# Performance work log

Measured on AMD Instinct MI355X. Metric: run time of the kernel, lower is better.

Reference implementation:

```python
import jax, jax.numpy as jnp
import numpy as np

EPS = 1e-5
N_HEADS = 32
TEMPERATURE = 1.0


def _inorm(x, g, b):
    # InstanceNorm2d (affine): normalize over H,W per (N, C)
    m = jnp.mean(x, axis=(-2, -1), keepdims=True)
    v = jnp.var(x, axis=(-2, -1), keepdims=True)
    return (x - m) * jax.lax.rsqrt(v + EPS) * g + b


def _resample(x, out_hw):
    # Fourier (spectral) resampling, matching neuraloperator's resample for skips
    H, W = x.shape[-2:]
    Ho, Wo = out_hw
    if (H, W) == (Ho, Wo):
        return x
    xf = jnp.fft.rfft2(x, norm='forward')
    kh = min(H, Ho) // 2
    kw = min(W // 2 + 1, Wo // 2 + 1)
    of = jnp.zeros(x.shape[:-2] + (Ho, Wo // 2 + 1), dtype=xf.dtype)
    of = of.at[..., :kh, :kw].set(xf[..., :kh, :kw])
    of = of.at[..., -kh:, :kw].set(xf[..., -kh:, :kw])
    return jnp.fft.irfft2(of, s=(Ho, Wo), norm='forward')


def _spec_conv(x, w, out_hw):
    # w: [2(pos/neg rows), in, out, m1, m2, 2(re/im)]; fft_norm='forward'
    m1, m2 = w.shape[3], w.shape[4]
    Ho, Wo = out_hw
    wc = w[..., 0] + 1j * w[..., 1]  # [2, in, out, m1, m2]
    xf = jnp.fft.rfft2(x, norm='forward')  # [B, Cin, H, W//2+1]
    top = jnp.einsum('bimn,iomn->bomn', xf[:, :, :m1, :m2], wc[0])
    bot = jnp.einsum('bimn,iomn->bomn', xf[:, :, -m1:, :m2], wc[1])
    of = jnp.zeros((x.shape[0], w.shape[2], Ho, Wo // 2 + 1), dtype=xf.dtype)
    of = of.at[:, :, :m1, :m2].set(top)
    of = of.at[:, :, -m1:, :m2].set(bot)
    return jnp.fft.irfft2(of, s=(Ho, Wo), norm='forward')


def _fno_layer(x, w, ws, bs, out_hw, norm_gb=None, act=False):
    # one FNOBlock layer: spectral conv + linear (1x1) skip, optional instance norm + gelu
    skip = jnp.einsum('bchw,oc->bohw', x, ws) + bs[None, :, None, None]
    skip = _resample(skip, out_hw)
    fno = _spec_conv(x, w, out_hw)
    if norm_gb is not None:
        fno = _inorm(fno, norm_gb[0], norm_gb[1])
    y = fno + skip
    if act:
        y = jax.nn.gelu(y, approximate=False)  # torch F.gelu default = exact erf
    return y


def _forward(x, wK, wKs, bKs, wQ, wQs, bQs, wV, wVs, bVs, wP, wPs, bPs,
             wM0, wM0s, bM0s, wM1, wM1s, bM1s, norm_g, norm_b):
    B, T, H, W = x.shape  # token_codimension == 1 -> tokens T == channels
    xa = x.reshape(B * T, 1, H, W)
    xa_n = _inorm(xa, norm_g[0], norm_b[0])  # self.norm1
    # K, Q at half resolution (output_scaling_factor = 1/scale, scale = 2); V at full res
    k = _fno_layer(xa_n, wK, wKs, bKs, (H // 2, W // 2))
    q = _fno_layer(xa_n, wQ, wQs, bQs, (H // 2, W // 2))
    v = _fno_layer(xa_n, wV, wVs, bVs, (H, W))

    def to_seq(z):
        h, w = z.shape[-2:]
        z = z.reshape(B, T, N_HEADS, 1, h, w).transpose(0, 2, 1, 3, 4, 5)
        return z.reshape(B, N_HEADS, T, h * w)  # d = head_codim = 1

    qs, ks, vs = to_seq(q), to_seq(k), to_seq(v)
    scores = jnp.einsum('bhtd,bhsd->bhts', qs, ks) / (np.sqrt(ks.shape[-1]).astype(np.float32) * TEMPERATURE)
    attn_w = jax.nn.softmax(scores, axis=-1)
    out = jnp.einsum('bhts,bhsd->bhtd', attn_w, vs)  # [B, heads, T, H*W]
    out = out.reshape(B, N_HEADS, T, 1, H, W).transpose(0, 2, 1, 3, 4, 5)
    out = out.reshape(B * T, N_HEADS, H, W)
    # proj: n_heads*head_codim != token_codim -> FNO projection back to 1 channel
    projd = _fno_layer(out, wP, wPs, bPs, (H, W))
    attention = _inorm(projd + xa, norm_g[1], norm_b[1])  # attention_normalizer
    an = _inorm(attention, norm_g[2], norm_b[2])  # self.norm2
    # permutation-equivariant mixer: 2 FNO layers, instance_norm, gelu between layers
    m = _fno_layer(an, wM0, wM0s, bM0s, (H, W), (norm_g[3], norm_b[3]), act=True)
    m = _fno_layer(m, wM1, wM1s, bM1s, (H, W), (norm_g[4], norm_b[4]), act=False)
    output = _inorm(m, norm_g[5], norm_b[5]) + attention  # mixer_out_normalizer + residual
    return output.reshape(B, T, H, W)


def setup_inputs() -> dict:
    key = jax.random.key(0)
    ks = jax.random.split(key, 16)
    B, T, H, W, heads = 2, 32, 128, 128, 32

    def rn(k, shape, s=1.0):
        return jax.random.normal(k, shape, jnp.float32) * s

    inp = {'x': rn(ks[0], (B, T, H, W))}
    for i, nm in enumerate(['K', 'Q', 'V']):
        inp['w' + nm] = rn(ks[1 + 3 * i], (2, 1, heads, 16, 16, 2), 1.0 / heads)
        inp['w' + nm + 's'] = rn(ks[2 + 3 * i], (heads, 1), 1.0)
        inp['b' + nm + 's'] = jnp.zeros((heads,), jnp.float32)
    inp['wP'] = rn(ks[10], (2, heads, 1, 32, 32, 2), 1.0 / heads)
    inp['wPs'] = rn(ks[11], (1, heads), 1.0 / heads)
    inp['bPs'] = jnp.zeros((1,), jnp.float32)
    inp['wM0'] = rn(ks[12], (2, 1, 1, 32, 32, 2), 1.0)
    inp['wM0s'] = rn(ks[13], (1, 1), 1.0)
    inp['bM0s'] = jnp.zeros((1,), jnp.float32)
    inp['wM1'] = rn(ks[14], (2, 1, 1, 32, 32, 2), 1.0)
    inp['wM1s'] = rn(ks[15], (1, 1), 1.0)
    inp['bM1s'] = jnp.zeros((1,), jnp.float32)
    inp['norm_g'] = jnp.ones((6,), jnp.float32)
    inp['norm_b'] = jnp.zeros((6,), jnp.float32)
    return inp


def reference(x, wK, wKs, bKs, wQ, wQs, bQs, wV, wVs, bVs, wP, wPs, bPs,
              wM0, wM0s, bM0s, wM1, wM1s, bM1s, norm_g, norm_b):
    return _forward(x, wK, wKs, bKs, wQ, wQs, bQs, wV, wVs, bVs, wP, wPs, bPs,
                    wM0, wM0s, bM0s, wM1, wM1s, bM1s, norm_g, norm_b)
```

## Files before the change

kernel.cpp:

```cpp
#include <hip/hip_runtime.h>
#include <math.h>


#define EPSV 1e-5f
#define PI2 6.283185307179586f

typedef float2 cf;

__device__ __forceinline__ cf cmul(cf a, cf b){ return make_float2(a.x*b.x - a.y*b.y, a.x*b.y + a.y*b.x); }
__device__ __forceinline__ cf ldc(const float* p){ return make_float2(p[0], p[1]); }
__device__ __forceinline__ void stc(float* p, cf v){ p[0]=v.x; p[1]=v.y; }

__device__ __forceinline__ void init_tw(cf* tw, int N, float dir){
  for (int j = threadIdx.x; j < N; j += blockDim.x){
    float s, c; sincosf(dir * PI2 * (float)j / (float)N, &s, &c);
    tw[j] = make_float2(c, s);
  }
}

__device__ void breduce2(float& a, float& b){
  __shared__ float sha[8], shb[8];
  for (int off = 32; off > 0; off >>= 1){
    a += __shfl_down(a, off, 64);
    b += __shfl_down(b, off, 64);
  }
  int w = threadIdx.x >> 6, lane = threadIdx.x & 63;
  int nw = (blockDim.x + 63) >> 6;
  if (lane == 0){ sha[w] = a; shb[w] = b; }
  __syncthreads();
  if (threadIdx.x == 0){
    for (int i = 1; i < nw; ++i){ a += sha[i]; b += shb[i]; }
    sha[0] = a; shb[0] = b;
  }
  __syncthreads();
  a = sha[0]; b = shb[0];
  __syncthreads();
}

__device__ __forceinline__ cf kq_mode(const float* w, int o, int kh, int kw){
  if (kw < 16){
    if (kh < 16)  return ldc(w + ((o*16+kh)*16+kw)*2);
    if (kh >= 48) return ldc(w + (((32+o)*16+(kh-48))*16+kw)*2);
  }
  return make_float2(0.f,0.f);
}

__global__ __launch_bounds__(256) void k_gamma_xstats(
                      const float* __restrict__ wQ, const float* __restrict__ wQs,
                      const float* __restrict__ bQs,
                      const float* __restrict__ wK, const float* __restrict__ wKs,
                      const float* __restrict__ bKs,
                      const float* __restrict__ x, const float* __restrict__ ng,
                      const float* __restrict__ nb,
                      float* __restrict__ gam, float* __restrict__ gcons,
                      float* __restrict__ stats, float* __restrict__ normAB){
  if (blockIdx.x >= 32){
    int n = blockIdx.x - 32;
    const float* im = x + n*16384;
    float s=0.f, s2=0.f;
    for (int i=threadIdx.x;i<16384;i+=256){ float v=im[i]; s+=v; s2=fmaf(v,v,s2); }
    breduce2(s,s2);
    if (threadIdx.x==0){
      float m = s*(1.f/16384.f), var = s2*(1.f/16384.f)-m*m;
      float A = rsqrtf(var+EPSV)*ng[0];
      normAB[n*2]=A; normAB[n*2+1]=nb[0]-m*A;
    }
    return;
  }
  int o = blockIdx.x;
  if (o==0){ for (int i=threadIdx.x;i<512;i+=256) stats[i]=0.f; }
  float sQ=wQs[o], sK=wKs[o];
  for (int m = threadIdx.x; m < 2112; m += 256){
    int kh = m/33, kw = m-kh*33;
    cf g;
    if (kw == 0){
      int mh = (64-kh)&63;
      cf qp = kq_mode(wQ,o,kh,0);  qp.x += sQ;
      cf qm = kq_mode(wQ,o,mh,0);  qm.x += sQ;
      cf qt = make_float2(0.5f*(qp.x+qm.x), 0.5f*(qp.y-qm.y));
      cf kp = kq_mode(wK,o,kh,0);  kp.x += sK;
      cf km = kq_mode(wK,o,mh,0);  km.x += sK;
      cf kt = make_float2(0.5f*(kp.x+km.x), 0.5f*(kp.y-km.y));
      g = make_float2(64.f*(qt.x*kt.x + qt.y*kt.y), 64.f*(qt.y*kt.x - qt.x*kt.y));
    } else if (kw == 32){
      g = make_float2(64.f*sQ*sK, 0.f);
    } else {
      cf q = kq_mode(wQ,o,kh,kw); q.x += sQ;
      cf k = kq_mode(wK,o,kh,kw); k.x += sK;
      g = make_float2(128.f*(q.x*k.x + q.y*k.y), 128.f*(q.y*k.x - q.x*k.y));
    }
    stc(gam + (o*2112+m)*2, g);
  }
  if (threadIdx.x == 0){
    float qt0 = sQ + kq_mode(wQ,o,0,0).x;
    float kt0 = sK + kq_mode(wK,o,0,0).x;
    gcons[o]    = 64.f*bKs[o]*qt0;
    gcons[32+o] = 64.f*bQs[o]*kt0;
    gcons[64+o] = 64.f*bQs[o]*bKs[o];
  }
}

__global__ __launch_bounds__(256) void k_rfft_row_x(const float* __restrict__ x, const float* __restrict__ normAB,
                                                    float* __restrict__ Cw){
  __shared__ float tile[16][128];
  __shared__ cf tw[128];
  init_tw(tw, 128, -1.f);
  int n = blockIdx.x, h0 = blockIdx.y*16;
  float A = normAB[n*2], Bc = normAB[n*2+1];
  for (int i=threadIdx.x;i<2048;i+=256) tile[i>>7][i&127] = fmaf(x[n*16384 + h0*128 + i], A, Bc);
  __syncthreads();
  for (int i=threadIdx.x;i<1024;i+=256){
    int hl=i>>6, w=i&63;
    float a=tile[hl][w], b=tile[hl][w+64];
    tile[hl][w]=a+b; tile[hl][w+64]=a-b;
  }
  __syncthreads();
  int hl = threadIdx.x >> 4, kws = threadIdx.x & 15;
  for (int kw=kws; kw<33; kw+=16){
    int sel = (kw&1)? 64 : 0;
    float re=0.f, im=0.f; int idx=0;
    for (int w=0;w<64;++w){
      float v=tile[hl][sel+w]; cf t=tw[idx];
      re=fmaf(v,t.x,re); im=fmaf(v,t.y,im);
      idx=(idx+kw)&127;
    }
    float* d = Cw + (((n*128)+(h0+hl))*33 + kw)*2;
    d[0]=re*(1.f/16384.f); d[1]=im*(1.f/16384.f);
  }
}

__global__ __launch_bounds__(256) void k_fcol(const float* __restrict__ Cw, float* __restrict__ F){
  __shared__ cf col[4][128];
  __shared__ cf tw[128];
  init_tw(tw, 128, -1.f);
  int n = blockIdx.x, kwb = blockIdx.y*4;
  for (int i=threadIdx.x;i<512;i+=256){
    int kwl=i>>7, h=i&127; int kw=kwb+kwl;
    col[kwl][h] = (kw<33) ? ldc(Cw + ((n*128+h)*33+kw)*2) : make_float2(0.f,0.f);
  }
  __syncthreads();
  {
    int i = threadIdx.x;
    int kwl = i>>6, h = i&63;
    cf a = col[kwl][h], b = col[kwl][h+64];
    col[kwl][h]    = make_float2(a.x+b.x, a.y+b.y);
    col[kwl][h+64] = make_float2(a.x-b.x, a.y-b.y);
  }
  __syncthreads();
  int r = threadIdx.x & 63, kwl = threadIdx.x >> 6;
  int kw = kwb + kwl;
  if (kw >= 33) return;
  int R = (r<32)? r : r+64;
  int sel = (r&1)? 64 : 0;
  float re=0.f, im=0.f; int idx=0;
  for (int j=0;j<64;++j){
    cf v=col[kwl][sel+j]; cf t=tw[idx];
    re = fmaf(v.x,t.x,re); re = fmaf(-v.y,t.y,re);
    im = fmaf(v.x,t.y,im); im = fmaf(v.y,t.x,im);
    idx=(idx+R)&127;
  }
  stc(F + ((n*64+r)*33+kw)*2, make_float2(re,im));
}

__global__ __launch_bounds__(256) void k_score(const float* __restrict__ F, const float* __restrict__ gam,
                                               float* __restrict__ scoreP){
  __shared__ float2 Esh[66][33];
  __shared__ float2 gsh[4][66];
  int mk = blockIdx.x, b = blockIdx.y, og = blockIdx.z;
  int m0 = mk*66;
  int t = threadIdx.x >> 3, s4 = (threadIdx.x & 7) << 2;
  for (int i = threadIdx.x; i < 2112; i += 256){
    int tt = i/66, j = i - tt*66;
    int m = m0 + j;
    int kh = m/33, kw = m - kh*33;
    const float* Fb = F + (b*32+tt)*4224;
    float2 v;
    if (kw < 32) v = *(const float2*)(Fb + (kh*33+kw)*2);
    else {
      int mh = (64-kh)&63;
      float2 a = *(const float2*)(Fb + (kh*33+32)*2);
      float2 c = *(const float2*)(Fb + (mh*33+32)*2);
      v = make_float2(0.5f*(a.x+c.x), 0.5f*(a.y-c.y));
    }
    Esh[j][tt] = v;
  }
  for (int i = threadIdx.x; i < 264; i += 256){
    int ol = i/66, j = i - ol*66;
    gsh[ol][j] = *(const float2*)(gam + ((og*4+ol)*2112 + m0 + j)*2);
  }
  __syncthreads();
  float acc[4][4];
  #pragma unroll
  for (int a=0;a<4;++a) for (int k=0;k<4;++k) acc[a][k]=0.f;
  #pragma unroll 2
  for (int j=0;j<66;++j){
    float2 et = Esh[j][t];
    float2 e0 = Esh[j][s4+0];
    float2 e1 = Esh[j][s4+1];
    float2 e2 = Esh[j][s4+2];
    float2 e3 = Esh[j][s4+3];
    #pragma unroll
    for (int ol=0;ol<4;++ol){
      float2 g = gsh[ol][j];
      float a  = g.x*et.x - g.y*et.y;
      float bb = g.x*et.y + g.y*et.x;
      acc[ol][0] = fmaf(a,e0.x,fmaf(bb,e0.y,acc[ol][0]));
      acc[ol][1] = fmaf(a,e1.x,fmaf(bb,e1.y,acc[ol][1]));
      acc[ol][2] = fmaf(a,e2.x,fmaf(bb,e2.y,acc[ol][2]));
      acc[ol][3] = fmaf(a,e3.x,fmaf(bb,e3.y,acc[ol][3]));
    }
  }
  #pragma unroll
  for (int ol=0;ol<4;++ol){
    int o = og*4+ol;
    float* sp = scoreP + (((mk*2+b)*32+o)*32 + t)*32 + s4;
    sp[0]=acc[ol][0]; sp[1]=acc[ol][1]; sp[2]=acc[ol][2]; sp[3]=acc[ol][3];
  }
}

__global__ __launch_bounds__(1024) void k_softmax(float* __restrict__ attn, const float* __restrict__ F,
                                                const float* __restrict__ gcons, const float* __restrict__ scoreP){
  __shared__ float Ssh[32][33];
  int b = blockIdx.x, o = blockIdx.y;
  int t = threadIdx.x >> 5, s = threadIdx.x & 31;
  float c0=gcons[o], c1=gcons[32+o], c2=gcons[64+o];
  float sc = c0*F[(b*32+t)*4224] + c1*F[(b*32+s)*4224] + c2;
  #pragma unroll 8
  for (int p=0;p<32;++p) sc += scoreP[(((p*2+b)*32+o)*32 + t)*32 + s];
  Ssh[t][s] = sc;
  __syncthreads();
  float mx = -1e30f;
  for (int ss=0;ss<32;++ss) mx = fmaxf(mx, Ssh[t][ss]);
  float e = expf(sc - mx);
  __syncthreads();
  Ssh[t][s] = e;
  __syncthreads();
  float sum = 0.f;
  for (int ss=0;ss<32;++ss) sum += Ssh[t][ss];
  attn[(b*32+o)*1024 + t*32 + s] = e/sum;
}

__device__ __forceinline__ cf wcV_col0(const float* wV, int o, int fr){
  if (fr < 16)  return ldc(wV + ((o*16+fr)*16)*2);
  if (fr >= 112) return ldc(wV + (((32+o)*16+(fr-112))*16)*2);
  return make_float2(0.f,0.f);
}

__global__ __launch_bounds__(256) void k_pmode(const float* __restrict__ F, const float* __restrict__ attn,
                        const float* __restrict__ wV, const float* __restrict__ wVs,
                        const float* __restrict__ wP, const float* __restrict__ wPs,
                        float* __restrict__ Pm){
  __shared__ float att[32][8][32];
  __shared__ cf Fsh[32][32];
  __shared__ cf dsh[32][32];
  int b = blockIdx.x, mh = blockIdx.y, tg = blockIdx.z;
  int fr = mh<32 ? mh : mh+64;
  int half = (mh>=32)?1:0, mr = mh&31;
  for (int i=threadIdx.x; i<8192; i+=256){
    int o = i>>8, r = i&255;
    att[o][r>>5][r&31] = attn[(b*32+o)*1024 + tg*256 + r];
  }
  for (int i=threadIdx.x; i<1024; i+=256){
    int s=i>>5, kw=i&31;
    Fsh[s][kw] = ldc(F + (((b*32+s)*64+mh)*33+kw)*2);
  }
  for (int i=threadIdx.x; i<1024; i+=256){
    int o=i>>5, kw=i&31;
    cf wp = ldc(wP + (((half*32+o)*32+mr)*32+kw)*2);
    cf bP = make_float2(wPs[o]+wp.x, wp.y);
    cf aV = make_float2(wVs[o], 0.f);
    if (kw==0){
      cf w1 = wcV_col0(wV,o,fr);
      cf w2 = wcV_col0(wV,o,(128-fr)&127);
      aV.x += 0.5f*(w1.x + w2.x);
      aV.y += 0.5f*(w1.y - w2.y);
    } else if (kw<16){
      if (fr<16){ cf wv=ldc(wV + ((o*16+fr)*16+kw)*2); aV.x+=wv.x; aV.y+=wv.y; }
      else if (fr>=112){ cf wv=ldc(wV + (((32+o)*16+(fr-112))*16+kw)*2); aV.x+=wv.x; aV.y+=wv.y; }
    }
    cf c = cmul(bP, aV);
    c.x -= wPs[o]*wVs[o];
    dsh[o][kw]=c;
  }
  __syncthreads();
  int tl = threadIdx.x>>5, kw = threadIdx.x&31;
  float ax=0.f, ay=0.f;
  for (int o=0;o<32;++o){
    float er=0.f, ei=0.f;
    #pragma unroll
    for (int s4=0;s4<32;s4+=4){
      float4 a4 = *(const float4*)&att[o][tl][s4];
      cf f0=Fsh[s4][kw], f1=Fsh[s4+1][kw], f2=Fsh[s4+2][kw], f3=Fsh[s4+3][kw];
      er=fmaf(a4.x,f0.x,er); ei=fmaf(a4.x,f0.y,ei);
      er=fmaf(a4.y,f1.x,er); ei=fmaf(a4.y,f1.y,ei);
      er=fmaf(a4.z,f2.x,er); ei=fmaf(a4.z,f2.y,ei);
      er=fmaf(a4.w,f3.x,er); ei=fmaf(a4.w,f3.y,ei);
    }
    cf d = dsh[o][kw];
    ax += d.x*er - d.y*ei;
    ay += d.x*ei + d.y*er;
  }
  int t = tg*8+tl;
  stc(Pm + ((b*32+t)*2048 + mh*32+kw)*2, make_float2(ax,ay));
}

__global__ __launch_bounds__(256) void k_zmix(const float* __restrict__ x, const float* __restrict__ Pm,
                        const float* __restrict__ attn, const float* __restrict__ normAB,
                        const float* __restrict__ wVs, const float* __restrict__ wPs,
                        const float* __restrict__ wP, const float* __restrict__ bPs,
                        const float* __restrict__ bVs,
                        float* __restrict__ z, float* __restrict__ stats){
  __shared__ cf Pmsh[64][33];
  __shared__ cf PmAsh[16][33];
  __shared__ float Mrow[32];
  __shared__ float cpart[33];
  __shared__ float consts;
  __shared__ cf tw[128];
  init_tw(tw, 128, 1.f);
  int n = blockIdx.x, b = n>>5, t = n&31, hb = blockIdx.y*8;
  for (int i=threadIdx.x;i<2048;i+=256)
    Pmsh[i>>5][i&31] = ldc(Pm + (n*2048 + i)*2);
  if (threadIdx.x < 32){
    int s = threadIdx.x;
    float a=0.f;
    for (int o=0;o<32;++o) a = fmaf(attn[(b*32+o)*1024 + t*32 + s], wVs[o]*wPs[o], a);
    float AxS = normAB[(b*32+s)*2], BcS = normAB[(b*32+s)*2+1];
    Mrow[s] = fmaf(a, AxS, (s==t)?1.f:0.f);
    cpart[s] = a*BcS;
  } else if (threadIdx.x == 32){
    float dcx = bPs[0];
    for (int o=0;o<32;++o){
      cf wp = ldc(wP + (o*1024)*2);
      dcx += (wPs[o]+wp.x)*bVs[o];
    }
    cpart[32] = dcx;
  }
  __syncthreads();
  if (threadIdx.x == 0){
    float c=0.f;
    for (int i=0;i<33;++i) c += cpart[i];
    consts = c;
  }
  {
    int bl = threadIdx.x>>5, kw = threadIdx.x&31;
    int h = hb + bl;
    float ser=0.f, sei=0.f, sor=0.f, soi=0.f;
    int s2h = (2*h)&127;
    int idx = 0;
    for (int khi=0;khi<32;khi+=2){
      cf v=Pmsh[khi][kw]; cf tt=tw[idx];
      ser += v.x*tt.x - v.y*tt.y; sei += v.x*tt.y + v.y*tt.x;
      idx=(idx+s2h)&127;
    }
    idx = (96*h)&127;
    for (int khi=32;khi<64;khi+=2){
      cf v=Pmsh[khi][kw]; cf tt=tw[idx];
      ser += v.x*tt.x - v.y*tt.y; sei += v.x*tt.y + v.y*tt.x;
      idx=(idx+s2h)&127;
    }
    idx = h&127;
    for (int khi=1;khi<32;khi+=2){
      cf v=Pmsh[khi][kw]; cf tt=tw[idx];
      sor += v.x*tt.x - v.y*tt.y; soi += v.x*tt.y + v.y*tt.x;
      idx=(idx+s2h)&127;
    }
    idx = (97*h)&127;
    for (int khi=33;khi<64;khi+=2){
      cf v=Pmsh[khi][kw]; cf tt=tw[idx];
      sor += v.x*tt.x - v.y*tt.y; soi += v.x*tt.y + v.y*tt.x;
      idx=(idx+s2h)&127;
    }
    PmAsh[bl][kw]   = make_float2(ser+sor, sei+soi);
    PmAsh[8+bl][kw] = make_float2(ser-sor, sei-soi);
  }
  __syncthreads();
  float cst = consts;
  float s1=0.f, s2=0.f;
  const float* xb = x + b*32*16384;
  {
    int hl = threadIdx.x>>4, wg = threadIdx.x&15;
    int w0 = wg*4;
    int gh = (hl<8)? hb+hl : hb+(hl-8)+64;
    int off = gh*128;
    float Se[4], So[4];
    #pragma unroll
    for (int j=0;j<4;++j){
      int w = w0+j;
      int s2w = (2*w)&127;
      float se=0.f, so=0.f;
      int idx=0;
      for (int kwp=0;kwp<16;++kwp){
        cf v = PmAsh[hl][2*kwp]; cf tt=tw[idx];
        float term = v.x*tt.x - v.y*tt.y;
        se += (kwp? 2.f:1.f)*term;
        idx=(idx+s2w)&127;
      }
      idx = w&127;
      for (int kwp=0;kwp<16;++kwp){
        cf v = PmAsh[hl][2*kwp+1]; cf tt=tw[idx];
        so += 2.f*(v.x*tt.x - v.y*tt.y);
        idx=(idx+s2w)&127;
      }
      Se[j]=se; So[j]=so;
    }
    float mixa[4]={0,0,0,0}, mixb[4]={0,0,0,0};
    for (int s=0;s<32;++s){
      float m = Mrow[s];
      float4 xa = *(const float4*)(xb + s*16384 + off + w0);
      float4 xc = *(const float4*)(xb + s*16384 + off + w0 + 64);
      mixa[0]=fmaf(m,xa.x,mixa[0]); mixa[1]=fmaf(m,xa.y,mixa[1]);
      mixa[2]=fmaf(m,xa.z,mixa[2]); mixa[3]=fmaf(m,xa.w,mixa[3]);
      mixb[0]=fmaf(m,xc.x,mixb[0]); mixb[1]=fmaf(m,xc.y,mixb[1]);
      mixb[2]=fmaf(m,xc.z,mixb[2]); mixb[3]=fmaf(m,xc.w,mixb[3]);
    }
    float oa[4], ob[4];
    #pragma unroll
    for (int j=0;j<4;++j){
      oa[j] = cst + Se[j] + So[j] + mixa[j];
      ob[j] = cst + Se[j] - So[j] + mixb[j];
      s1 += oa[j]+ob[j];
      s2 += oa[j]*oa[j] + ob[j]*ob[j];
    }
    *(float4*)(z + n*16384 + off + w0)      = make_float4(oa[0],oa[1],oa[2],oa[3]);
    *(float4*)(z + n*16384 + off + w0 + 64) = make_float4(ob[0],ob[1],ob[2],ob[3]);
  }
  breduce2(s1,s2);
  if (threadIdx.x==0){ atomicAdd(&stats[n*2],s1); atomicAdd(&stats[n*2+1],s2); }
}

__global__ __launch_bounds__(256) void k_rfft_row_an(const float* __restrict__ z, const float* __restrict__ statsZ,
                              const float* __restrict__ ng, const float* __restrict__ nb,
                              float* __restrict__ Tm){
  __shared__ float tile[16][128];
  __shared__ cf tw[128];
  init_tw(tw,128,-1.f);
  int n=blockIdx.x, h0=blockIdx.y*16;
  float S=statsZ[n*2], S2=statsZ[n*2+1];
  float mz=S*(1.f/16384.f), vz=S2*(1.f/16384.f)-mz*mz;
  float az=rsqrtf(vz+EPSV);
  float g1=ng[1], g2=ng[2], b2v=nb[2];
  float vat = g1*g1*vz*az*az;
  float C1 = az*g1*rsqrtf(vat+EPSV)*g2;
  float Dc = b2v - mz*C1;
  for (int i=threadIdx.x;i<2048;i+=256)
    tile[i>>7][i&127] = fmaf(z[n*16384+h0*128+i], C1, Dc);
  __syncthreads();
  for (int i=threadIdx.x;i<1024;i+=256){
    int hl=i>>6, w=i&63;
    float a=tile[hl][w], b=tile[hl][w+64];
    tile[hl][w]=a+b; tile[hl][w+64]=a-b;
  }
  __syncthreads();
  for (int i=threadIdx.x;i<512;i+=256){
    int hl=i>>5, kw=i&31;
    int sel = (kw&1)? 64 : 0;
    float re=0.f,im=0.f; int idx=0;
    for (int w=0;w<64;++w){
      float v=tile[hl][sel+w]; cf t=tw[idx];
      re=fmaf(v,t.x,re); im=fmaf(v,t.y,im);
      idx=(idx+kw)&127;
    }
    float* d = Tm + ((n*128+h0+hl)*32+kw)*2;
    d[0]=re*(1.f/16384.f); d[1]=im*(1.f/16384.f);
  }
}

__global__ __launch_bounds__(256) void k_colpair(const float* __restrict__ Tm, const float* __restrict__ wM,
                                                 float* __restrict__ Am){
  __shared__ cf Tsh[128][9];
  __shared__ cf Gsh[64][9];
  __shared__ cf tw[128];
  init_tw(tw,128,-1.f);
  int n = blockIdx.x, kw8 = blockIdx.y*8;
  for (int i=threadIdx.x;i<1024;i+=256){
    int h=i>>3, kwl=i&7;
    Tsh[h][kwl] = ldc(Tm + ((n*128+h)*32 + kw8+kwl)*2);
  }
  __syncthreads();
  for (int i=threadIdx.x;i<512;i+=256){
    int h=i>>3, kwl=i&7;
    cf a=Tsh[h][kwl], b=Tsh[h+64][kwl];
    Tsh[h][kwl]    = make_float2(a.x+b.x, a.y+b.y);
    Tsh[h+64][kwl] = make_float2(a.x-b.x, a.y-b.y);
  }
  __syncthreads();
  {
    int kwl = threadIdx.x&7, base = threadIdx.x>>3;
    for (int r=0;r<2;++r){
      int khi = r*32 + base;
      int khF = (khi<32)? khi : khi+64;
      int sel = (khi&1)? 64 : 0;
      float re=0.f, im=0.f; int idx=0;
      for (int j=0;j<64;++j){
        cf v=Tsh[sel+j][kwl]; cf t=tw[idx];
        re += v.x*t.x - v.y*t.y; im += v.x*t.y + v.y*t.x;
        idx=(idx+khF)&127;
      }
      int half=(khi>=32)?1:0, mr=khi&31;
      cf wv = ldc(wM + ((half*32+mr)*32 + kw8+kwl)*2);
      Gsh[khi][kwl] = cmul(make_float2(re,im), wv);
    }
  }
  __syncthreads();
  {
    int kwl = threadIdx.x&7, base = threadIdx.x>>3;
    for (int r=0;r<2;++r){
      int h = r*32 + base;
      float ser=0.f, sei=0.f, sor=0.f, soi=0.f;
      int s2h = (2*h)&127;
      int idx=0;
      for (int khi=0;khi<32;khi+=2){
        cf v=Gsh[khi][kwl]; cf t=tw[idx];
        ser += v.x*t.x + v.y*t.y; sei += v.y*t.x - v.x*t.y;
        idx=(idx+s2h)&127;
      }
      idx=(96*h)&127;
      for (int khi=32;khi<64;khi+=2){
        cf v=Gsh[khi][kwl]; cf t=tw[idx];
        ser += v.x*t.x + v.y*t.y; sei += v.y*t.x - v.x*t.y;
        idx=(idx+s2h)&127;
      }
      idx=h&127;
      for (int khi=1;khi<32;khi+=2){
        cf v=Gsh[khi][kwl]; cf t=tw[idx];
        sor += v.x*t.x + v.y*t.y; soi += v.y*t.x - v.x*t.y;
        idx=(idx+s2h)&127;
      }
      idx=(97*h)&127;
      for (int khi=33;khi<64;khi+=2){
        cf v=Gsh[khi][kwl]; cf t=tw[idx];
        sor += v.x*t.x + v.y*t.y; soi += v.y*t.x - v.x*t.y;
        idx=(idx+s2h)&127;
      }
      stc(Am + ((n*128+h)*32 + kw8+kwl)*2,    make_float2(ser+sor, sei+soi));
      stc(Am + ((n*128+h+64)*32 + kw8+kwl)*2, make_float2(ser-sor, sei-soi));
    }
  }
}

__global__ __launch_bounds__(256) void k_mirfft_row(const float* __restrict__ Am, float* __restrict__ out,
                                                    float* __restrict__ stats){
  __shared__ cf rowA[16][33];
  __shared__ cf tw[128];
  init_tw(tw,128,1.f);
  int n=blockIdx.x, h0=blockIdx.y*16;
  for (int i=threadIdx.x;i<512;i+=256){
    int hl=i>>5, kw=i&31;
    rowA[hl][kw] = ldc(Am + ((n*128+h0+hl)*32+kw)*2);
  }
  __syncthreads();
  float s=0.f,s2=0.f;
  for (int i=threadIdx.x;i<1024;i+=256){
    int hl=i>>6, w=i&63;
    int s2w = (2*w)&127;
    float se=0.f, so=0.f;
    int idx=0;
    for (int kwp=0;kwp<16;++kwp){
      cf v=rowA[hl][2*kwp]; cf t=tw[idx];
      float term=v.x*t.x-v.y*t.y;
      se += (kwp? 2.f:1.f)*term;
      idx=(idx+s2w)&127;
    }
    idx = w&127;
    for (int kwp=0;kwp<16;++kwp){
      cf v=rowA[hl][2*kwp+1]; cf t=tw[idx];
      so += 2.f*(v.x*t.x-v.y*t.y);
      idx=(idx+s2w)&127;
    }
    float oa = se+so, ob = se-so;
    out[n*16384+(h0+hl)*128+w]    = oa;
    out[n*16384+(h0+hl)*128+w+64] = ob;
    s+=oa+ob; s2 += oa*oa + ob*ob;
  }
  breduce2(s,s2);
  if (threadIdx.x==0){ atomicAdd(&stats[n*2],s); atomicAdd(&stats[n*2+1],s2); }
}

__global__ __launch_bounds__(256) void k_m0_rfft_row(const float* __restrict__ fno, const float* __restrict__ z,
                              const float* __restrict__ stats0, const float* __restrict__ statsZ,
                              const float* __restrict__ ng, const float* __restrict__ nb,
                              const float* __restrict__ wM0s, const float* __restrict__ bM0s,
                              float* __restrict__ m0out, float* __restrict__ Tm){
  __shared__ float tile[16][128];
  __shared__ cf tw[128];
  init_tw(tw,128,-1.f);
  int n=blockIdx.x, h0=blockIdx.y*16;
  float S0=stats0[n*2], S02=stats0[n*2+1];
  float m0m=S0*(1.f/16384.f), v0=S02*(1.f/16384.f)-m0m*m0m;
  float A0=rsqrtf(v0+EPSV)*ng[3];
  float B0=nb[3]-m0m*A0;
  float Sz=statsZ[n*2], Sz2=statsZ[n*2+1];
  float mz=Sz*(1.f/16384.f), vz=Sz2*(1.f/16384.f)-mz*mz;
  float az=rsqrtf(vz+EPSV);
  float g1=ng[1], g2=ng[2];
  float vat=g1*g1*vz*az*az;
  float C1=az*g1*rsqrtf(vat+EPSV)*g2;
  float Dc=nb[2]-mz*C1;
  float ws_=wM0s[0], bs_=bM0s[0];
  for (int i=threadIdx.x;i<2048;i+=256){
    int gi = n*16384 + h0*128 + i;
    float nf = fmaf(fno[gi], A0, B0);
    float an = fmaf(z[gi], C1, Dc);
    float pre = nf + fmaf(ws_, an, bs_);
    float gv = 0.5f*pre*(1.f+erff(pre*0.70710678118654752f));
    tile[i>>7][i&127]=gv;
    m0out[gi]=gv;
  }
  __syncthreads();
  for (int i=threadIdx.x;i<1024;i+=256){
    int hl=i>>6, w=i&63;
    float a=tile[hl][w], b=tile[hl][w+64];
    tile[hl][w]=a+b; tile[hl][w+64]=a-b;
  }
  __syncthreads();
  for (int i=threadIdx.x;i<512;i+=256){
    int hl=i>>5, kw=i&31;
    int sel = (kw&1)? 64:0;
    float re=0.f,im=0.f; int idx=0;
    for (int w=0;w<64;++w){
      float v=tile[hl][sel+w]; cf t=tw[idx];
      re=fmaf(v,t.x,re); im=fmaf(v,t.y,im);
      idx=(idx+kw)&127;
    }
    float* d = Tm + ((n*128+h0+hl)*32+kw)*2;
    d[0]=re*(1.f/16384.f); d[1]=im*(1.f/16384.f);
  }
}

__global__ __launch_bounds__(256) void k_m1_mix(const float* fno1, const float* __restrict__ m0,
                         const float* __restrict__ stats1, const float* __restrict__ ng, const float* __restrict__ nb,
                         const float* __restrict__ wM1s, const float* __restrict__ bM1s,
                         float* m1out, float* __restrict__ stats2){
  int n=blockIdx.x, h0=blockIdx.y*16;
  float S=stats1[n*2], S2v=stats1[n*2+1];
  float m1m=S*(1.f/16384.f), v1=S2v*(1.f/16384.f)-m1m*m1m;
  float A1=rsqrtf(v1+EPSV)*ng[4];
  float Bc1=nb[4]-m1m*A1;
  float ws_=wM1s[0], bs_=bM1s[0];
  float s=0.f,s2=0.f;
  for (int i=threadIdx.x;i<2048;i+=256){
    int gi=n*16384+h0*128+i;
    float v = fmaf(fno1[gi],A1,Bc1) + fmaf(ws_,m0[gi],bs_);
    m1out[gi]=v;
    s+=v; s2=fmaf(v,v,s2);
  }
  breduce2(s,s2);
  if (threadIdx.x==0){ atomicAdd(&stats2[n*2],s); atomicAdd(&stats2[n*2+1],s2); }
}

__global__ __launch_bounds__(256) void k_final(const float* __restrict__ m1, const float* __restrict__ z,
                        const float* __restrict__ stats2, const float* __restrict__ statsZ,
                        const float* __restrict__ ng, const float* __restrict__ nb,
                        float* __restrict__ out){
  int n=blockIdx.x, h0=blockIdx.y*16;
  float S=stats2[n*2], S2v=stats2[n*2+1];
  float mm=S*(1.f/16384.f), vv=S2v*(1.f/16384.f)-mm*mm;
  float A2=rsqrtf(vv+EPSV)*ng[5];
  float B2c=nb[5]-mm*A2;
  float Sz=statsZ[n*2], Sz2=statsZ[n*2+1];
  float mz=Sz*(1.f/16384.f), vz=Sz2*(1.f/16384.f)-mz*mz;
  float Az=rsqrtf(vz+EPSV)*ng[1];
  float Bz=nb[1]-mz*Az;
  for (int i=threadIdx.x;i<2048;i+=256){
    int gi=n*16384+h0*128+i;
    out[gi] = fmaf(m1[gi],A2,B2c) + fmaf(z[gi],Az,Bz);
  }
}

extern "C" void kernel_launch(void* const* d_in, const int* in_sizes, int n_in,
                              void* d_out, int out_size, void* d_ws, size_t ws_size,
                              hipStream_t stream){
  (void)in_sizes; (void)n_in; (void)out_size; (void)ws_size;
  const float* x   = (const float*)d_in[0];
  const float* wK  = (const float*)d_in[1];
  const float* wKs = (const float*)d_in[2];
  const float* bKs = (const float*)d_in[3];
  const float* wQ  = (const float*)d_in[4];
  const float* wQs = (const float*)d_in[5];
  const float* bQs = (const float*)d_in[6];
  const float* wV  = (const float*)d_in[7];
  const float* wVs = (const float*)d_in[8];
  const float* bVs = (const float*)d_in[9];
  const float* wP  = (const float*)d_in[10];
  const float* wPs = (const float*)d_in[11];
  const float* bPs = (const float*)d_in[12];
  const float* wM0 = (const float*)d_in[13];
  const float* wM0s= (const float*)d_in[14];
  const float* bM0s= (const float*)d_in[15];
  const float* wM1 = (const float*)d_in[16];
  const float* wM1s= (const float*)d_in[17];
  const float* bM1s= (const float*)d_in[18];
  const float* ng  = (const float*)d_in[19];
  const float* nb  = (const float*)d_in[20];
  float* out = (float*)d_out;
  float* ws  = (float*)d_ws;

  float* F      = ws;
  float* Cw     = F + 270336;
  float* scoreP = Cw + 540672;
  float* attn   = scoreP + 2097152;
  float* stats  = attn + 65536;
  float* Pm     = stats + 512;
  float* gcons  = Pm + 262144;
  float* gam    = gcons + 128;
  float* normAB = gam + 135168;
  float* z      = normAB + 128;
  float* m0b    = z + 1048576;
  float* fx     = m0b + 1048576;
  float* Tm     = fx + 1048576;
  float* Am     = Tm + 524288;
  float* statsZ = stats;
  float* stats0 = stats + 128;
  float* stats1 = stats + 256;
  float* stats2 = stats + 384;

  k_gamma_xstats<<<96,256,0,stream>>>(wQ,wQs,bQs, wK,wKs,bKs, x, ng, nb, gam, gcons, stats, normAB);
  k_rfft_row_x<<<dim3(64,8),256,0,stream>>>(x, normAB, Cw);
  k_fcol<<<dim3(64,9),256,0,stream>>>(Cw, F);
  k_score<<<dim3(32,2,8),256,0,stream>>>(F, gam, scoreP);
  k_softmax<<<dim3(2,32),1024,0,stream>>>(attn, F, gcons, scoreP);
  k_pmode<<<dim3(2,64,4),256,0,stream>>>(F, attn, wV, wVs, wP, wPs, Pm);
  k_zmix<<<dim3(64,8),256,0,stream>>>(x, Pm, attn, normAB, wVs, wPs, wP, bPs, bVs, z, statsZ);
  k_rfft_row_an<<<dim3(64,8),256,0,stream>>>(z, statsZ, ng, nb, Tm);
  k_colpair<<<dim3(64,4),256,0,stream>>>(Tm, wM0, Am);
  k_mirfft_row<<<dim3(64,8),256,0,stream>>>(Am, fx, stats0);
  k_m0_rfft_row<<<dim3(64,8),256,0,stream>>>(fx, z, stats0, statsZ, ng, nb, wM0s, bM0s, m0b, Tm);
  k_colpair<<<dim3(64,4),256,0,stream>>>(Tm, wM1, Am);
  k_mirfft_row<<<dim3(64,8),256,0,stream>>>(Am, fx, stats1);
  k_m1_mix<<<dim3(64,8),256,0,stream>>>(fx, m0b, stats1, ng, nb, wM1s, bM1s, fx, stats2);
  k_final<<<dim3(64,8),256,0,stream>>>(fx, z, stats2, statsZ, ng, nb, out);
}
```

Baseline: 261.3 us.

## Fuse forward 2D FFT, fold row FFT into zmix, compute final norm stats analytically

Merges the row and column forward FFTs into a single 1024-thread kernel per image that keeps the intermediate in shared memory, so the Cw workspace round trip goes away. The row DFT of z moves into k_zmix, and the instance-norm affine is applied in the spectral domain inside k_colpair, which removes k_rfft_row_an. The k_m1_mix pass is dropped by deriving the second norm's mean and variance from sums of f1 and m0 plus a cross term gathered in the existing passes. This cuts launches and global traffic, but k_fwd2d runs only 64 blocks, so GPU occupancy is low, and the algebraic variance formula may lose some precision.

```diff
diff --git a/kernel.cpp b/kernel.cpp
--- a/kernel.cpp
+++ b/kernel.cpp
@@ -19,7 +19,7 @@
 }
 
 __device__ void breduce2(float& a, float& b){
-  __shared__ float sha[8], shb[8];
+  __shared__ float sha[16], shb[16];
   for (int off = 32; off > 0; off >>= 1){
     a += __shfl_down(a, off, 64);
     b += __shfl_down(b, off, 64);
@@ -68,7 +68,7 @@
     return;
   }
   int o = blockIdx.x;
-  if (o==0){ for (int i=threadIdx.x;i<512;i+=256) stats[i]=0.f; }
+  if (o==0){ for (int i=threadIdx.x;i<640;i+=256) stats[i]=0.f; }
   float sQ=wQs[o], sK=wKs[o];
   for (int m = threadIdx.x; m < 2112; m += 256){
     int kh = m/33, kw = m-kh*33;
@@ -100,66 +100,54 @@
   }
 }
 
-__global__ __launch_bounds__(256) void k_rfft_row_x(const float* __restrict__ x, const float* __restrict__ normAB,
-                                                    float* __restrict__ Cw){
-  __shared__ float tile[16][128];
+__global__ __launch_bounds__(1024) void k_fwd2d(const float* __restrict__ x, const float* __restrict__ normAB,
+                                                float* __restrict__ F){
+  __shared__ float zb[16384];
+  __shared__ cf Crow[4224];
   __shared__ cf tw[128];
   init_tw(tw, 128, -1.f);
-  int n = blockIdx.x, h0 = blockIdx.y*16;
+  int n = blockIdx.x;
   float A = normAB[n*2], Bc = normAB[n*2+1];
-  for (int i=threadIdx.x;i<2048;i+=256) tile[i>>7][i&127] = fmaf(x[n*16384 + h0*128 + i], A, Bc);
-  __syncthreads();
-  for (int i=threadIdx.x;i<1024;i+=256){
-    int hl=i>>6, w=i&63;
-    float a=tile[hl][w], b=tile[hl][w+64];
-    tile[hl][w]=a+b; tile[hl][w+64]=a-b;
-  }
-  __syncthreads();
-  int hl = threadIdx.x >> 4, kws = threadIdx.x & 15;
-  for (int kw=kws; kw<33; kw+=16){
+  for (int i=threadIdx.x;i<16384;i+=1024) zb[i] = fmaf(x[n*16384+i], A, Bc);
+  __syncthreads();
+  for (int i=threadIdx.x;i<8192;i+=1024){
+    int h=i>>6, w=i&63;
+    float a=zb[h*128+w], b=zb[h*128+w+64];
+    zb[h*128+w]=a+b; zb[h*128+w+64]=a-b;
+  }
+  __syncthreads();
+  for (int i=threadIdx.x;i<4224;i+=1024){
+    int h=i/33, kw=i-h*33;
     int sel = (kw&1)? 64 : 0;
     float re=0.f, im=0.f; int idx=0;
     for (int w=0;w<64;++w){
-      float v=tile[hl][sel+w]; cf t=tw[idx];
+      float v=zb[h*128+sel+w]; cf t=tw[idx];
       re=fmaf(v,t.x,re); im=fmaf(v,t.y,im);
       idx=(idx+kw)&127;
     }
-    float* d = Cw + (((n*128)+(h0+hl))*33 + kw)*2;
-    d[0]=re*(1.f/16384.f); d[1]=im*(1.f/16384.f);
-  }
-}
-
-__global__ __launch_bounds__(256) void k_fcol(const float* __restrict__ Cw, float* __restrict__ F){
-  __shared__ cf col[4][128];
-  __shared__ cf tw[128];
-  init_tw(tw, 128, -1.f);
-  int n = blockIdx.x, kwb = blockIdx.y*4;
-  for (int i=threadIdx.x;i<512;i+=256){
-    int kwl=i>>7, h=i&127; int kw=kwb+kwl;
-    col[kwl][h] = (kw<33) ? ldc(Cw + ((n*128+h)*33+kw)*2) : make_float2(0.f,0.f);
-  }
-  __syncthreads();
-  {
-    int i = threadIdx.x;
-    int kwl = i>>6, h = i&63;
-    cf a = col[kwl][h], b = col[kwl][h+64];
-    col[kwl][h]    = make_float2(a.x+b.x, a.y+b.y);
-    col[kwl][h+64] = make_float2(a.x-b.x, a.y-b.y);
-  }
-  __syncthreads();
-  int r = threadIdx.x & 63, kwl = threadIdx.x >> 6;
-  int kw = kwb + kwl;
-  if (kw >= 33) return;
-  int R = (r<32)? r : r+64;
-  int sel = (r&1)? 64 : 0;
-  float re=0.f, im=0.f; int idx=0;
-  for (int j=0;j<64;++j){
-    cf v=col[kwl][sel+j]; cf t=tw[idx];
-    re = fmaf(v.x,t.x,re); re = fmaf(-v.y,t.y,re);
-    im = fmaf(v.x,t.y,im); im = fmaf(v.y,t.x,im);
-    idx=(idx+R)&127;
-  }
-  stc(F + ((n*64+r)*33+kw)*2, make_float2(re,im));
+    Crow[i] = make_float2(re*(1.f/16384.f), im*(1.f/16384.f));
+  }
+  __syncthreads();
+  for (int i=threadIdx.x;i<2112;i+=1024){
+    int h=i/33, kw=i-h*33;
+    cf a=Crow[h*33+kw], b=Crow[(h+64)*33+kw];
+    Crow[h*33+kw]      = make_float2(a.x+b.x, a.y+b.y);
+    Crow[(h+64)*33+kw] = make_float2(a.x-b.x, a.y-b.y);
+  }
+  __syncthreads();
+  for (int i=threadIdx.x;i<2112;i+=1024){
+    int r=i/33, kw=i-r*33;
+    int R = (r<32)? r : r+64;
+    int sel = (r&1)? 64 : 0;
+    float re=0.f, im=0.f; int idx=0;
+    for (int j=0;j<64;++j){
+      cf v=Crow[(sel+j)*33+kw]; cf t=tw[idx];
+      re = fmaf(v.x,t.x,re); re = fmaf(-v.y,t.y,re);
+      im = fmaf(v.x,t.y,im); im = fmaf(v.y,t.x,im);
+      idx=(idx+R)&127;
+    }
+    stc(F + ((n*64+r)*33+kw)*2, make_float2(re,im));
+  }
 }
 
 __global__ __launch_bounds__(256) void k_score(const float* __restrict__ F, const float* __restrict__ gam,
@@ -309,9 +297,11 @@
                         const float* __restrict__ wVs, const float* __restrict__ wPs,
                         const float* __restrict__ wP, const float* __restrict__ bPs,
                         const float* __restrict__ bVs,
-                        float* __restrict__ z, float* __restrict__ stats){
+                        float* __restrict__ z, float* __restrict__ stats,
+                        float* __restrict__ Tm){
   __shared__ cf Pmsh[64][33];
   __shared__ cf PmAsh[16][33];
+  __shared__ float zrows[16][128];
   __shared__ float Mrow[32];
   __shared__ float cpart[33];
   __shared__ float consts;
@@ -420,61 +410,61 @@
       ob[j] = cst + Se[j] - So[j] + mixb[j];
       s1 += oa[j]+ob[j];
       s2 += oa[j]*oa[j] + ob[j]*ob[j];
+      zrows[hl][w0+j]    = oa[j];
+      zrows[hl][w0+64+j] = ob[j];
     }
     *(float4*)(z + n*16384 + off + w0)      = make_float4(oa[0],oa[1],oa[2],oa[3]);
     *(float4*)(z + n*16384 + off + w0 + 64) = make_float4(ob[0],ob[1],ob[2],ob[3]);
   }
+  __syncthreads();
+  for (int i=threadIdx.x;i<1024;i+=256){
+    int hl=i>>6, w=i&63;
+    float a=zrows[hl][w], bz=zrows[hl][w+64];
+    zrows[hl][w]=a+bz; zrows[hl][w+64]=a-bz;
+  }
+  __syncthreads();
+  for (int i=threadIdx.x;i<512;i+=256){
+    int hl=i>>5, kw=i&31;
+    int gh = (hl<8)? hb+hl : hb+(hl-8)+64;
+    int sel = (kw&1)? 64 : 0;
+    float re=0.f, im=0.f; int idx=0;
+    for (int w=0;w<64;++w){
+      float v=zrows[hl][sel+w]; cf tt=tw[idx];
+      re=fmaf(v,tt.x,re); im=fmaf(v,tt.y,im);
+      idx=(idx+kw)&127;
+    }
+    float* d = Tm + ((n*128+gh)*32+kw)*2;
+    d[0]=re*(1.f/16384.f); d[1]=-im*(1.f/16384.f);
+  }
   breduce2(s1,s2);
   if (threadIdx.x==0){ atomicAdd(&stats[n*2],s1); atomicAdd(&stats[n*2+1],s2); }
 }
 
-__global__ __launch_bounds__(256) void k_rfft_row_an(const float* __restrict__ z, const float* __restrict__ statsZ,
-                              const float* __restrict__ ng, const float* __restrict__ nb,
-                              float* __restrict__ Tm){
-  __shared__ float tile[16][128];
-  __shared__ cf tw[128];
-  init_tw(tw,128,-1.f);
-  int n=blockIdx.x, h0=blockIdx.y*16;
-  float S=statsZ[n*2], S2=statsZ[n*2+1];
-  float mz=S*(1.f/16384.f), vz=S2*(1.f/16384.f)-mz*mz;
-  float az=rsqrtf(vz+EPSV);
-  float g1=ng[1], g2=ng[2], b2v=nb[2];
-  float vat = g1*g1*vz*az*az;
-  float C1 = az*g1*rsqrtf(vat+EPSV)*g2;
-  float Dc = b2v - mz*C1;
-  for (int i=threadIdx.x;i<2048;i+=256)
-    tile[i>>7][i&127] = fmaf(z[n*16384+h0*128+i], C1, Dc);
-  __syncthreads();
-  for (int i=threadIdx.x;i<1024;i+=256){
-    int hl=i>>6, w=i&63;
-    float a=tile[hl][w], b=tile[hl][w+64];
-    tile[hl][w]=a+b; tile[hl][w+64]=a-b;
-  }
-  __syncthreads();
-  for (int i=threadIdx.x;i<512;i+=256){
-    int hl=i>>5, kw=i&31;
-    int sel = (kw&1)? 64 : 0;
-    float re=0.f,im=0.f; int idx=0;
-    for (int w=0;w<64;++w){
-      float v=tile[hl][sel+w]; cf t=tw[idx];
-      re=fmaf(v,t.x,re); im=fmaf(v,t.y,im);
-      idx=(idx+kw)&127;
-    }
-    float* d = Tm + ((n*128+h0+hl)*32+kw)*2;
-    d[0]=re*(1.f/16384.f); d[1]=im*(1.f/16384.f);
-  }
-}
-
 __global__ __launch_bounds__(256) void k_colpair(const float* __restrict__ Tm, const float* __restrict__ wM,
-                                                 float* __restrict__ Am){
+                                                 const float* __restrict__ statsZ,
+                                                 const float* __restrict__ ng, const float* __restrict__ nb,
+                                                 int apply_an, float* __restrict__ Am){
   __shared__ cf Tsh[128][9];
   __shared__ cf Gsh[64][9];
   __shared__ cf tw[128];
   init_tw(tw,128,-1.f);
   int n = blockIdx.x, kw8 = blockIdx.y*8;
+  float C1 = 1.f, Dc128 = 0.f;
+  if (apply_an){
+    float S=statsZ[n*2], S2=statsZ[n*2+1];
+    float mz=S*(1.f/16384.f), vz=S2*(1.f/16384.f)-mz*mz;
+    float az=rsqrtf(vz+EPSV);
+    float g1=ng[1], g2=ng[2];
+    float vat = g1*g1*vz*az*az;
+    C1 = az*g1*rsqrtf(vat+EPSV)*g2;
+    Dc128 = (nb[2] - mz*C1)*(1.f/128.f);
+  }
   for (int i=threadIdx.x;i<1024;i+=256){
     int h=i>>3, kwl=i&7;
-    Tsh[h][kwl] = ldc(Tm + ((n*128+h)*32 + kw8+kwl)*2);
+    cf v = ldc(Tm + ((n*128+h)*32 + kw8+kwl)*2);
+    v.x *= C1; v.y *= C1;
+    if (apply_an && (kw8+kwl)==0) v.x += Dc128;
+    Tsh[h][kwl] = v;
   }
   __syncthreads();
   for (int i=threadIdx.x;i<512;i+=256){
@@ -539,7 +529,9 @@
 }
 
 __global__ __launch_bounds__(256) void k_mirfft_row(const float* __restrict__ Am, float* __restrict__ out,
-                                                    float* __restrict__ stats){
+                                                    float* __restrict__ stats,
+                                                    const float* __restrict__ m0, float* __restrict__ statsC,
+                                                    int withCross){
   __shared__ cf rowA[16][33];
   __shared__ cf tw[128];
   init_tw(tw,128,1.f);
@@ -549,7 +541,7 @@
     rowA[hl][kw] = ldc(Am + ((n*128+h0+hl)*32+kw)*2);
   }
   __syncthreads();
-  float s=0.f,s2=0.f;
+  float s=0.f,s2=0.f,s3=0.f;
   for (int i=threadIdx.x;i<1024;i+=256){
     int hl=i>>6, w=i&63;
     int s2w = (2*w)&127;
@@ -568,19 +560,30 @@
       idx=(idx+s2w)&127;
     }
     float oa = se+so, ob = se-so;
-    out[n*16384+(h0+hl)*128+w]    = oa;
-    out[n*16384+(h0+hl)*128+w+64] = ob;
+    int gi = n*16384+(h0+hl)*128+w;
+    out[gi]    = oa;
+    out[gi+64] = ob;
     s+=oa+ob; s2 += oa*oa + ob*ob;
+    if (withCross){
+      s3 = fmaf(oa, m0[gi], s3);
+      s3 = fmaf(ob, m0[gi+64], s3);
+    }
   }
   breduce2(s,s2);
   if (threadIdx.x==0){ atomicAdd(&stats[n*2],s); atomicAdd(&stats[n*2+1],s2); }
+  if (withCross){
+    float d=0.f;
+    breduce2(s3,d);
+    if (threadIdx.x==0) atomicAdd(&statsC[n*2],s3);
+  }
 }
 
 __global__ __launch_bounds__(256) void k_m0_rfft_row(const float* __restrict__ fno, const float* __restrict__ z,
                               const float* __restrict__ stats0, const float* __restrict__ statsZ,
                               const float* __restrict__ ng, const float* __restrict__ nb,
                               const float* __restrict__ wM0s, const float* __restrict__ bM0s,
-                              float* __restrict__ m0out, float* __restrict__ Tm){
+                              float* __restrict__ m0out, float* __restrict__ Tm,
+                              float* __restrict__ statsM0){
   __shared__ float tile[16][128];
   __shared__ cf tw[128];
   init_tw(tw,128,-1.f);
@@ -597,6 +600,7 @@
   float C1=az*g1*rsqrtf(vat+EPSV)*g2;
   float Dc=nb[2]-mz*C1;
   float ws_=wM0s[0], bs_=bM0s[0];
+  float sm=0.f, sm2=0.f;
   for (int i=threadIdx.x;i<2048;i+=256){
     int gi = n*16384 + h0*128 + i;
     float nf = fmaf(fno[gi], A0, B0);
@@ -605,6 +609,7 @@
     float gv = 0.5f*pre*(1.f+erff(pre*0.70710678118654752f));
     tile[i>>7][i&127]=gv;
     m0out[gi]=gv;
+    sm+=gv; sm2=fmaf(gv,gv,sm2);
   }
   __syncthreads();
   for (int i=threadIdx.x;i<1024;i+=256){
@@ -625,45 +630,38 @@
     float* d = Tm + ((n*128+h0+hl)*32+kw)*2;
     d[0]=re*(1.f/16384.f); d[1]=im*(1.f/16384.f);
   }
-}
-
-__global__ __launch_bounds__(256) void k_m1_mix(const float* fno1, const float* __restrict__ m0,
-                         const float* __restrict__ stats1, const float* __restrict__ ng, const float* __restrict__ nb,
-                         const float* __restrict__ wM1s, const float* __restrict__ bM1s,
-                         float* m1out, float* __restrict__ stats2){
+  breduce2(sm,sm2);
+  if (threadIdx.x==0){ atomicAdd(&statsM0[n*2],sm); atomicAdd(&statsM0[n*2+1],sm2); }
+}
+
+__global__ __launch_bounds__(256) void k_final(const float* __restrict__ f1, const float* __restrict__ m0,
+                        const float* __restrict__ z,
+                        const float* __restrict__ stats1, const float* __restrict__ statsM0,
+                        const float* __restrict__ statsC, const float* __restrict__ statsZ,
+                        const float* __restrict__ ng, const float* __restrict__ nb,
+                        const float* __restrict__ wM1s, const float* __restrict__ bM1s,
+                        float* __restrict__ out){
   int n=blockIdx.x, h0=blockIdx.y*16;
-  float S=stats1[n*2], S2v=stats1[n*2+1];
-  float m1m=S*(1.f/16384.f), v1=S2v*(1.f/16384.f)-m1m*m1m;
+  const float N = 16384.f, iN = 1.f/16384.f;
+  float Sf=stats1[n*2], Sf2=stats1[n*2+1];
+  float m1m=Sf*iN, v1=Sf2*iN-m1m*m1m;
   float A1=rsqrtf(v1+EPSV)*ng[4];
   float Bc1=nb[4]-m1m*A1;
-  float ws_=wM1s[0], bs_=bM1s[0];
-  float s=0.f,s2=0.f;
+  float ws_=wM1s[0], K=Bc1+bM1s[0];
+  float Sm=statsM0[n*2], Sm2=statsM0[n*2+1], Sfm=statsC[n*2];
+  float S1m = A1*Sf + ws_*Sm + N*K;
+  float S2m = A1*A1*Sf2 + ws_*ws_*Sm2 + N*K*K + 2.f*A1*ws_*Sfm + 2.f*A1*K*Sf + 2.f*ws_*K*Sm;
+  float mean2 = S1m*iN, var2 = S2m*iN - mean2*mean2;
+  float A2=rsqrtf(var2+EPSV)*ng[5];
+  float B2c=nb[5]-mean2*A2;
+  float Sz=statsZ[n*2], Sz2=statsZ[n*2+1];
+  float mz=Sz*iN, vz=Sz2*iN-mz*mz;
+  float Az=rsqrtf(vz+EPSV)*ng[1];
+  float Bz=nb[1]-mz*Az;
+  float cf1 = A2*A1, cm0 = A2*ws_, cc = A2*K + B2c;
   for (int i=threadIdx.x;i<2048;i+=256){
     int gi=n*16384+h0*128+i;
-    float v = fmaf(fno1[gi],A1,Bc1) + fmaf(ws_,m0[gi],bs_);
-    m1out[gi]=v;
-    s+=v; s2=fmaf(v,v,s2);
-  }
-  breduce2(s,s2);
-  if (threadIdx.x==0){ atomicAdd(&stats2[n*2],s); atomicAdd(&stats2[n*2+1],s2); }
-}
-
-__global__ __launch_bounds__(256) void k_final(const float* __restrict__ m1, const float* __restrict__ z,
-                        const float* __restrict__ stats2, const float* __restrict__ statsZ,
-                        const float* __restrict__ ng, const float* __restrict__ nb,
-                        float* __restrict__ out){
-  int n=blockIdx.x, h0=blockIdx.y*16;
-  float S=stats2[n*2], S2v=stats2[n*2+1];
-  float mm=S*(1.f/16384.f), vv=S2v*(1.f/16384.f)-mm*mm;
-  float A2=rsqrtf(vv+EPSV)*ng[5];
-  float B2c=nb[5]-mm*A2;
-  float Sz=statsZ[n*2], Sz2=statsZ[n*2+1];
-  float mz=Sz*(1.f/16384.f), vz=Sz2*(1.f/16384.f)-mz*mz;
-  float Az=rsqrtf(vz+EPSV)*ng[1];
-  float Bz=nb[1]-mz*Az;
-  for (int i=threadIdx.x;i<2048;i+=256){
-    int gi=n*16384+h0*128+i;
-    out[gi] = fmaf(m1[gi],A2,B2c) + fmaf(z[gi],Az,Bz);
+    out[gi] = fmaf(f1[gi],cf1, fmaf(m0[gi],cm0, cc)) + fmaf(z[gi],Az,Bz);
   }
 }
 
@@ -696,11 +694,10 @@
   float* ws  = (float*)d_ws;
 
   float* F      = ws;
-  float* Cw     = F + 270336;
-  float* scoreP = Cw + 540672;
+  float* scoreP = F + 270336;
   float* attn   = scoreP + 2097152;
   float* stats  = attn + 65536;
-  float* Pm     = stats + 512;
+  float* Pm     = stats + 640;
   float* gcons  = Pm + 262144;
   float* gam    = gcons + 128;
   float* normAB = gam + 135168;
@@ -712,21 +709,19 @@
   float* statsZ = stats;
   float* stats0 = stats + 128;
   float* stats1 = stats + 256;
-  float* stats2 = stats + 384;
+  float* statsM0= stats + 384;
+  float* statsC = stats + 512;
 
   k_gamma_xstats<<<96,256,0,stream>>>(wQ,wQs,bQs, wK,wKs,bKs, x, ng, nb, gam, gcons, stats, normAB);
-  k_rfft_row_x<<<dim3(64,8),256,0,stream>>>(x, normAB, Cw);
-  k_fcol<<<dim3(64,9),256,0,stream>>>(Cw, F);
+  k_fwd2d<<<64,1024,0,stream>>>(x, normAB, F);
   k_score<<<dim3(32,2,8),256,0,stream>>>(F, gam, scoreP);
   k_softmax<<<dim3(2,32),1024,0,stream>>>(attn, F, gcons, scoreP);
   k_pmode<<<dim3(2,64,4),256,0,stream>>>(F, attn, wV, wVs, wP, wPs, Pm);
-  k_zmix<<<dim3(64,8),256,0,stream>>>(x, Pm, attn, normAB, wVs, wPs, wP, bPs, bVs, z, statsZ);
-  k_rfft_row_an<<<dim3(64,8),256,0,stream>>>(z, statsZ, ng, nb, Tm);
-  k_colpair<<<dim3(64,4),256,0,stream>>>(Tm, wM0, Am);
-  k_mirfft_row<<<dim3(64,8),256,0,stream>>>(Am, fx, stats0);
-  k_m0_rfft_row<<<dim3(64,8),256,0,stream>>>(fx, z, stats0, statsZ, ng, nb, wM0s, bM0s, m0b, Tm);
-  k_colpair<<<dim3(64,4),256,0,stream>>>(Tm, wM1, Am);
-  k_mirfft_row<<<dim3(64,8),256,0,stream>>>(Am, fx, stats1);
-  k_m1_mix<<<dim3(64,8),256,0,stream>>>(fx, m0b, stats1, ng, nb, wM1s, bM1s, fx, stats2);
-  k_final<<<dim3(64,8),256,0,stream>>>(fx, z, stats2, statsZ, ng, nb, out);
-}
+  k_zmix<<<dim3(64,8),256,0,stream>>>(x, Pm, attn, normAB, wVs, wPs, wP, bPs, bVs, z, statsZ, Tm);
+  k_colpair<<<dim3(64,4),256,0,stream>>>(Tm, wM0, statsZ, ng, nb, 1, Am);
+  k_mirfft_row<<<dim3(64,8),256,0,stream>>>(Am, fx, stats0, (const float*)nullptr, (float*)nullptr, 0);
+  k_m0_rfft_row<<<dim3(64,8),256,0,stream>>>(fx, z, stats0, statsZ, ng, nb, wM0s, bM0s, m0b, Tm, statsM0);
+  k_colpair<<<dim3(64,4),256,0,stream>>>(Tm, wM1, statsZ, ng, nb, 0, Am);
+  k_mirfft_row<<<dim3(64,8),256,0,stream>>>(Am, fx, stats1, m0b, statsC, 1);
+  k_final<<<dim3(64,8),256,0,stream>>>(fx, m0b, z, stats1, statsM0, statsC, statsZ, ng, nb, wM1s, bM1s, out);
+}
```

Result: slower. 271.2 us (+3.8%).
